# Kernel tuning notes

Measured on AMD Instinct MI355X. Metric: run time of the kernel, lower is better.

Reference implementation:

```python
import jax, jax.numpy as jnp
import numpy as np

N, S, C, E = 32768, 32768, 1024, 16384   # nodes, subgraph-node entries, clusters (=B*P), coarsen edges
F, D, B, P, NC = 64, 64, 16, 64, 10      # feat dim, hidden, graphs, patches per graph, classes


def setup_inputs():
    key = jax.random.key(0)
    ks = list(jax.random.split(key, 24))
    p = lambda k, shp: jax.random.normal(k, shp, dtype=jnp.float32) * 0.05
    z = lambda n: jnp.zeros((n,), jnp.float32)
    return {
        "x": jax.random.normal(ks[0], (N, F), dtype=jnp.float32),
        "subgraphs_nodes_mapper": jax.random.randint(ks[1], (S,), 0, N, dtype=jnp.int32),
        "subgraphs_batch": jnp.sort(jax.random.randint(ks[2], (S,), 0, C, dtype=jnp.int32)),
        "subgraphs_batch_row": jax.random.randint(ks[3], (E,), 0, C, dtype=jnp.int32),
        "subgraphs_batch_col": jax.random.randint(ks[4], (E,), 0, C, dtype=jnp.int32),
        "coarsen_edge_attr": jax.random.uniform(ks[5], (E,), dtype=jnp.float32),
        "W_in1": p(ks[6], (F, D)), "b_in1": z(D),
        "W_in2": p(ks[7], (D, D)), "b_in2": z(D),
        "W_pre1": p(ks[8], (D, D)), "b_pre1": z(D),
        "W_pre2": p(ks[9], (D, D)), "b_pre2": z(D),
        "W_post1": p(ks[10], (D, D)), "b_post1": z(D),
        "W_post2": p(ks[11], (D, D)), "b_post2": z(D),
        "W_K": p(ks[12], (D, D)), "b_K": z(D),
        "W_V": p(ks[13], (D, D)), "b_V": z(D),
        "alpha_beta": jax.random.normal(ks[14], (2,), dtype=jnp.float32),
        "W_c1": p(ks[15], (D, D // 2)), "b_c1": z(D // 2),
        "W_c2": p(ks[16], (D // 2, NC)), "b_c2": z(NC),
    }


def reference(x, subgraphs_nodes_mapper, subgraphs_batch, subgraphs_batch_row,
              subgraphs_batch_col, coarsen_edge_attr,
              W_in1, b_in1, W_in2, b_in2, W_pre1, b_pre1, W_pre2, b_pre2,
              W_post1, b_post1, W_post2, b_post2, W_K, b_K, W_V, b_V,
              alpha_beta, W_c1, b_c1, W_c2, b_c2):
    seg_sum = lambda v, idx: jax.ops.segment_sum(v, idx, num_segments=C)
    # input transform MLP (use_gnn=False path)
    h = jax.nn.relu(x @ W_in1 + b_in1)
    h = jax.nn.relu(h @ W_in2 + b_in2)
    sx = h[subgraphs_nodes_mapper]                        # [S, D] irregular gather
    b = subgraphs_batch
    row, col = subgraphs_batch_row, subgraphs_batch_col
    # bincount-based symmetric degree normalization of coarsened edge weights
    deg = seg_sum(coarsen_edge_attr, row)                 # [C]
    dinv = jnp.where(deg > 0, deg ** -0.5, 0.0)
    ea = dinv[row] * coarsen_edge_attr * dinv[col]        # [E]
    # Q path: pre-deepset -> scatter sum -> post-deepset
    Q = jax.nn.relu(sx @ W_pre1 + b_pre1) @ W_pre2 + b_pre2
    Qs = seg_sum(Q, b)
    Qs = jax.nn.relu(Qs @ W_post1 + b_post1) @ W_post2 + b_post2  # [C, D]
    # K / V paths
    K = sx @ W_K + b_K                                    # [S, D]
    cnt = jnp.maximum(seg_sum(jnp.ones((S,), sx.dtype), b), 1.0)
    Ks = seg_sum(K, b) / cnt[:, None]                     # scatter-mean [C, D]
    V = sx @ W_V + b_V                                    # [S, D]
    # relu kernelization
    Qk, Kk, Ksk = jax.nn.relu(Qs), jax.nn.relu(K), jax.nn.relu(Ks)
    ab = jax.nn.softmax(alpha_beta)
    sa, sb = ab[0] ** -0.5, ab[1] ** -0.5
    ck = jnp.concatenate([sa * Ksk[b], sb * Kk], axis=-1)   # [S, 2D]
    cq = jnp.concatenate([sa * Qk, sb * Qk], axis=-1)       # [C, 2D] (diffQ=False)
    ck_s = seg_sum(ck, b)                                   # [C, 2D]
    M = ck[:, :, None] * V[:, None, :]                      # [S, 2D, D] per-entry outer product
    Ms = seg_sum(M, b)                                      # [C, 2D, D]
    # Double_Level_MessageProp / KeyProp on coarsened graph: out[c] = sum_e ea_e * x[row_e] at col_e
    Ms = seg_sum(ea[:, None, None] * Ms[row], col)
    ck_s = seg_sum(ea[:, None] * ck_s[row], col)
    H = jnp.einsum('ci,cij->cj', cq, Ms)                    # [C, D]
    den = jnp.sum(cq * ck_s, axis=-1, keepdims=True) + 1e-6
    out = H / den                                           # [C, D]
    g = out.reshape(B, P, D).mean(axis=1)                   # mean readout over patches
    logits = jax.nn.relu(g @ W_c1 + b_c1) @ W_c2 + b_c2     # [B, NC]
    return logits
```

## Files before the change

kernel.cpp:

```cpp
#include <hip/hip_runtime.h>
#include <math.h>

constexpr int NN = 32768;
constexpr int SS = 32768;
constexpr int CC = 1024;
constexpr int EE = 16384;
constexpr int BB = 16;
constexpr int PP = 64;
constexpr int NC = 10;
constexpr int ECAP = 64;

__device__ __forceinline__ float rdlane(float v, int l) {
    return __int_as_float(__builtin_amdgcn_readlane(__float_as_int(v), l));
}

#define TS 68

__device__ __forceinline__ void gemm64(const float* A, const float* W,
                                       const float* __restrict__ bias,
                                       int r0, int c0, float acc[4][4])
{
#pragma unroll
    for (int dc = 0; dc < 4; ++dc) {
        float bv = bias[c0 + dc];
        acc[0][dc] = bv; acc[1][dc] = bv; acc[2][dc] = bv; acc[3][dc] = bv;
    }
#pragma unroll 16
    for (int k = 0; k < 64; ++k) {
        float4 av = *(const float4*)(A + k * TS + r0);
        float4 wv = *(const float4*)(W + k * TS + c0);
        acc[0][0] = fmaf(av.x, wv.x, acc[0][0]); acc[0][1] = fmaf(av.x, wv.y, acc[0][1]);
        acc[0][2] = fmaf(av.x, wv.z, acc[0][2]); acc[0][3] = fmaf(av.x, wv.w, acc[0][3]);
        acc[1][0] = fmaf(av.y, wv.x, acc[1][0]); acc[1][1] = fmaf(av.y, wv.y, acc[1][1]);
        acc[1][2] = fmaf(av.y, wv.z, acc[1][2]); acc[1][3] = fmaf(av.y, wv.w, acc[1][3]);
        acc[2][0] = fmaf(av.z, wv.x, acc[2][0]); acc[2][1] = fmaf(av.z, wv.y, acc[2][1]);
        acc[2][2] = fmaf(av.z, wv.z, acc[2][2]); acc[2][3] = fmaf(av.z, wv.w, acc[2][3]);
        acc[3][0] = fmaf(av.w, wv.x, acc[3][0]); acc[3][1] = fmaf(av.w, wv.y, acc[3][1]);
        acc[3][2] = fmaf(av.w, wv.z, acc[3][2]); acc[3][3] = fmaf(av.w, wv.w, acc[3][3]);
    }
}

__device__ __forceinline__ void gemm64x3(const float* A, const float* Wa,
                                         const float* Wb, const float* Wc_,
                                         const float* __restrict__ b1_,
                                         const float* __restrict__ b2_,
                                         const float* __restrict__ b3_,
                                         int r0, int c0,
                                         float a1_[4][4], float a2_[4][4], float a3_[4][4])
{
#pragma unroll
    for (int dc = 0; dc < 4; ++dc) {
        float v1 = b1_[c0 + dc], v2 = b2_[c0 + dc], v3 = b3_[c0 + dc];
#pragma unroll
        for (int dr = 0; dr < 4; ++dr) { a1_[dr][dc] = v1; a2_[dr][dc] = v2; a3_[dr][dc] = v3; }
    }
#pragma unroll 4
    for (int k = 0; k < 64; ++k) {
        float4 av = *(const float4*)(A + k * TS + r0);
        float4 w1 = *(const float4*)(Wa + k * TS + c0);
        float4 w2 = *(const float4*)(Wb + k * TS + c0);
        float4 w3 = *(const float4*)(Wc_ + k * TS + c0);
        float ar[4] = {av.x, av.y, av.z, av.w};
        float u1[4] = {w1.x, w1.y, w1.z, w1.w};
        float u2[4] = {w2.x, w2.y, w2.z, w2.w};
        float u3[4] = {w3.x, w3.y, w3.z, w3.w};
#pragma unroll
        for (int dr = 0; dr < 4; ++dr)
#pragma unroll
            for (int dc = 0; dc < 4; ++dc) {
                a1_[dr][dc] = fmaf(ar[dr], u1[dc], a1_[dr][dc]);
                a2_[dr][dc] = fmaf(ar[dr], u2[dc], a2_[dr][dc]);
                a3_[dr][dc] = fmaf(ar[dr], u3[dc], a3_[dr][dc]);
            }
    }
}

__device__ __forceinline__ void writeW(float* dst, int tid,
                                       float4 a, float4 b, float4 c, float4 d)
{
    int colq = (tid & 15) * 4;
    int rb = tid >> 4;
    *(float4*)(dst + (rb     ) * TS + colq) = a;
    *(float4*)(dst + (rb + 16) * TS + colq) = b;
    *(float4*)(dst + (rb + 32) * TS + colq) = c;
    *(float4*)(dst + (rb + 48) * TS + colq) = d;
}

__device__ __forceinline__ void writeXT(float* dst, int tid,
                                        float4 a, float4 b, float4 c, float4 d)
{
    int rb = (tid * 4) & 63;
    int cb = tid >> 4;
    dst[(rb + 0) * TS + cb     ] = a.x;
    dst[(rb + 1) * TS + cb     ] = a.y;
    dst[(rb + 2) * TS + cb     ] = a.z;
    dst[(rb + 3) * TS + cb     ] = a.w;
    dst[(rb + 0) * TS + cb + 16] = b.x;
    dst[(rb + 1) * TS + cb + 16] = b.y;
    dst[(rb + 2) * TS + cb + 16] = b.z;
    dst[(rb + 3) * TS + cb + 16] = b.w;
    dst[(rb + 0) * TS + cb + 32] = c.x;
    dst[(rb + 1) * TS + cb + 32] = c.y;
    dst[(rb + 2) * TS + cb + 32] = c.z;
    dst[(rb + 3) * TS + cb + 32] = c.w;
    dst[(rb + 0) * TS + cb + 48] = d.x;
    dst[(rb + 1) * TS + cb + 48] = d.y;
    dst[(rb + 2) * TS + cb + 48] = d.z;
    dst[(rb + 3) * TS + cb + 48] = d.w;
}

__device__ __forceinline__ void outT_relu(float* dst, int r0, int c0, float acc[4][4])
{
#pragma unroll
    for (int dc = 0; dc < 4; ++dc) {
        *(float4*)(dst + (c0 + dc) * TS + r0) =
            make_float4(fmaxf(acc[0][dc], 0.f), fmaxf(acc[1][dc], 0.f),
                        fmaxf(acc[2][dc], 0.f), fmaxf(acc[3][dc], 0.f));
    }
}

__device__ __forceinline__ void outG2(float* __restrict__ dst, size_t rowbase, int ld,
                                      int off, int r0, int c0, float acc[4][4], bool dorelu)
{
#pragma unroll
    for (int dr = 0; dr < 4; ++dr) {
        float4 v = make_float4(acc[dr][0], acc[dr][1], acc[dr][2], acc[dr][3]);
        if (dorelu) {
            v.x = fmaxf(v.x, 0.f); v.y = fmaxf(v.y, 0.f);
            v.z = fmaxf(v.z, 0.f); v.w = fmaxf(v.w, 0.f);
        }
        *(float4*)(dst + (rowbase + r0 + dr) * ld + off + c0) = v;
    }
}

__global__ __launch_bounds__(256, 2) void k_node(
    const float* __restrict__ x,
    const int* __restrict__ row, const float* __restrict__ attr,
    const int* __restrict__ batch,
    const float* __restrict__ W1, const float* __restrict__ b1,
    const float* __restrict__ W2, const float* __restrict__ b2,
    const float* __restrict__ Wp1, const float* __restrict__ bp1,
    const float* __restrict__ WK, const float* __restrict__ bK,
    const float* __restrict__ WV, const float* __restrict__ bV,
    float* __restrict__ u, float* __restrict__ KV,
    float* __restrict__ deg, int* __restrict__ segoff,
    int* __restrict__ gcnt, int* __restrict__ ebuck,
    float* __restrict__ zbase)
{
    __shared__ __align__(16) float bufA[64 * TS];
    __shared__ __align__(16) float bufB[64 * TS];
    __shared__ __align__(16) float w0[64 * TS];
    __shared__ __align__(16) float w1[64 * TS];
    __shared__ float ldeg[16];
    __shared__ int lbk[4];
    int tid = threadIdx.x;
    int b = blockIdx.x;
    if (tid < 33) {
        int i = b * 33 + tid;
        if (i < 16640) ((float4*)zbase)[i] = make_float4(0.f, 0.f, 0.f, 0.f);
    }
    if (b < 64) {
        if (tid < 16) ldeg[tid] = 0.f;
        __syncthreads();
        int lo = b * 16;
#pragma unroll 4
        for (int i = 0; i < 64; ++i) {
            int e = i * 256 + tid;
            int r = row[e];
            unsigned d = (unsigned)(r - lo);
            if (d < 16u) atomicAdd(&ldeg[d], attr[e]);
        }
        __syncthreads();
        if (tid < 16) deg[lo + tid] = ldeg[tid];
    } else if (b < 192) {
        int t = (b - 64) * 256 + tid;
        int cur = batch[t];
        int prev = (t == 0) ? -1 : batch[t - 1];
        for (int c = prev + 1; c <= cur; ++c) segoff[c] = t;
        if (t == SS - 1)
            for (int c = cur + 1; c <= CC; ++c) segoff[c] = SS;
    } else if (b < 448) {
        int crow = (b - 192) * 4;
        if (tid < 4) lbk[tid] = 0;
        __syncthreads();
#pragma unroll 4
        for (int i = 0; i < 64; ++i) {
            int e = i * 256 + tid;
            int r = row[e];
            unsigned d = (unsigned)(r - crow);
            if (d < 4u) {
                int pos = atomicAdd(&lbk[d], 1);
                if (pos < ECAP) ebuck[(size_t)(crow + d) * ECAP + pos] = e;
            }
        }
        __syncthreads();
        if (tid < 4) gcnt[crow + tid] = min(lbk[tid], ECAP);
    }
    int tx = tid & 15, ty = tid >> 4;
    int r0 = ty * 4, c0 = tx * 4;
    size_t rowbase = (size_t)b * 64;
    const float* xb = x + rowbase * 64;
    float4 a0 = ((const float4*)W1)[tid];
    float4 a1 = ((const float4*)W1)[tid + 256];
    float4 a2 = ((const float4*)W1)[tid + 512];
    float4 a3 = ((const float4*)W1)[tid + 768];
    float4 x0 = ((const float4*)xb)[tid];
    float4 x1 = ((const float4*)xb)[tid + 256];
    float4 x2 = ((const float4*)xb)[tid + 512];
    float4 x3 = ((const float4*)xb)[tid + 768];
    writeW(w0, tid, a0, a1, a2, a3);
    writeXT(bufA, tid, x0, x1, x2, x3);
    __syncthreads();
    float acc[4][4];
    a0 = ((const float4*)W2)[tid];
    a1 = ((const float4*)W2)[tid + 256];
    a2 = ((const float4*)W2)[tid + 512];
    a3 = ((const float4*)W2)[tid + 768];
    gemm64(bufA, w0, b1, r0, c0, acc);
    outT_relu(bufB, r0, c0, acc);
    writeW(w1, tid, a0, a1, a2, a3);
    __syncthreads();
    a0 = ((const float4*)Wp1)[tid];
    a1 = ((const float4*)Wp1)[tid + 256];
    a2 = ((const float4*)Wp1)[tid + 512];
    a3 = ((const float4*)Wp1)[tid + 768];
    float4 k0 = ((const float4*)WK)[tid];
    float4 k1 = ((const float4*)WK)[tid + 256];
    float4 k2 = ((const float4*)WK)[tid + 512];
    float4 k3 = ((const float4*)WK)[tid + 768];
    float4 v0 = ((const float4*)WV)[tid];
    float4 v1 = ((const float4*)WV)[tid + 256];
    float4 v2 = ((const float4*)WV)[tid + 512];
    float4 v3 = ((const float4*)WV)[tid + 768];
    gemm64(bufB, w1, b2, r0, c0, acc);
    outT_relu(bufA, r0, c0, acc);
    writeW(w0, tid, a0, a1, a2, a3);
    writeW(w1, tid, k0, k1, k2, k3);
    writeW(bufB, tid, v0, v1, v2, v3);
    __syncthreads();
    float accU[4][4], accK[4][4], accV[4][4];
    gemm64x3(bufA, w0, w1, bufB, bp1, bK, bV, r0, c0, accU, accK, accV);
    outG2(u, rowbase, 64, 0, r0, c0, accU, true);
    outG2(KV, rowbase, 128, 0, r0, c0, accK, false);
    outG2(KV, rowbase, 128, 64, r0, c0, accV, false);
}

__global__ __launch_bounds__(256, 4) void k_qk(
    const float* __restrict__ u, const int* __restrict__ mapper,
    const int* __restrict__ segoff,
    const float* __restrict__ Wp2, const float* __restrict__ bp2,
    const float* __restrict__ Wpo1, const float* __restrict__ bpo1,
    const float* __restrict__ Wpo2, const float* __restrict__ bpo2,
    float* __restrict__ Qk)
{
    __shared__ float accs[4][64];
    int c = blockIdx.x;
    int tid = threadIdx.x, j = tid & 63, g = tid >> 6;
    int s0 = segoff[c], s1 = segoff[c + 1];
    float L = (float)(s1 - s0);
    if (tid < 64) {
        accs[0][tid] = 0.f;
        accs[1][tid] = L * bp2[tid];
        accs[2][tid] = bpo1[tid];
        accs[3][tid] = bpo2[tid];
    }
    __syncthreads();
    float us = 0.f;
    for (int s = s0 + g; s < s1; s += 4) us += u[(size_t)mapper[s] * 64 + j];
    atomicAdd(&accs[0][j], us);
    __syncthreads();
    float usv = accs[0][j];
    float p = 0.f;
#pragma unroll
    for (int t = 0; t < 16; ++t) {
        int i = g * 16 + t;
        p = fmaf(rdlane(usv, i), Wp2[i * 64 + j], p);
    }
    atomicAdd(&accs[1][j], p);
    __syncthreads();
    float qs = accs[1][j];
    p = 0.f;
#pragma unroll
    for (int t = 0; t < 16; ++t) {
        int i = g * 16 + t;
        p = fmaf(rdlane(qs, i), Wpo1[i * 64 + j], p);
    }
    atomicAdd(&accs[2][j], p);
    __syncthreads();
    float tv = fmaxf(accs[2][j], 0.f);
    p = 0.f;
#pragma unroll
    for (int t = 0; t < 16; ++t) {
        int i = g * 16 + t;
        p = fmaf(rdlane(tv, i), Wpo2[i * 64 + j], p);
    }
    atomicAdd(&accs[3][j], p);
    __syncthreads();
    if (g == 0) Qk[c * 64 + j] = fmaxf(accs[3][j], 0.f);
}

#define KSTR 72
#define MSTR 68

__global__ __launch_bounds__(256, 4) void k_msbedge(
    const float* __restrict__ KV, const int* __restrict__ mapper,
    const int* __restrict__ segoff, const float* __restrict__ Qk,
    const int* __restrict__ col, const float* __restrict__ attr,
    const float* __restrict__ deg,
    const int* __restrict__ gcnt, const int* __restrict__ ebuck,
    const float* __restrict__ ab,
    float* __restrict__ H, float* __restrict__ den)
{
    __shared__ __align__(16) float Kr[32 * KSTR];
    __shared__ __align__(16) float Vb[32 * KSTR];
    __shared__ __align__(16) float msb[64 * MSTR];
    __shared__ int map_lds[32];
    __shared__ float sums[192];
    __shared__ float dvec[64];
    __shared__ int ecol[ECAP];
    __shared__ float ewt[ECAP];
    int c = blockIdx.x;
    int tid = threadIdx.x, j = tid & 63, g = tid >> 6;
    int tx = tid & 15, ty = tid >> 4;
    int r0 = ty * 4, c0 = tx * 4;
    int ne = gcnt[c];
    if (ne == 0) return;
    int nr = (ne + 15) & ~15;
    if (tid < 192) sums[tid] = 0.f;
    if (tid < ne) {
        int e = ebuck[(size_t)c * ECAP + tid];
        int cd = col[e];
        float dc = deg[cd];
        float dinvc = dc > 0.f ? 1.f / sqrtf(dc) : 0.f;
        float drr = deg[c];
        float dinvr = drr > 0.f ? 1.f / sqrtf(drr) : 0.f;
        ecol[tid] = cd;
        ewt[tid] = dinvr * attr[e] * dinvc;
    }
    for (int p = ne + tid; p < nr; p += 256) { ecol[p] = c; ewt[p] = 0.f; }
    int s0 = segoff[c], s1 = segoff[c + 1];
    float acc[4][4];
#pragma unroll
    for (int a = 0; a < 4; ++a)
#pragma unroll
        for (int bq = 0; bq < 4; ++bq) acc[a][bq] = 0.f;
    float ks = 0.f, krs = 0.f, vs = 0.f;
    for (int sb = s0; sb < s1; sb += 32) {
        int clen = min(32, s1 - sb);
        __syncthreads();
        if (tid < clen) map_lds[tid] = mapper[sb + tid];
        __syncthreads();
        for (int p = tid; p < clen * 32; p += 256) {
            int e = p >> 5, q = p & 31;
            int m = map_lds[e];
            float4 v = *(const float4*)(KV + (size_t)m * 128 + q * 4);
            float* dst = (q < 16) ? &Kr[e * KSTR + q * 4] : &Vb[e * KSTR + (q - 16) * 4];
            *(float4*)dst = v;
        }
        __syncthreads();
#pragma unroll 4
        for (int s = 0; s < clen; ++s) {
            float4 a4 = *(const float4*)(&Kr[s * KSTR + r0]);
            float4 b4 = *(const float4*)(&Vb[s * KSTR + c0]);
            float ar0 = fmaxf(a4.x, 0.f), ar1 = fmaxf(a4.y, 0.f);
            float ar2 = fmaxf(a4.z, 0.f), ar3 = fmaxf(a4.w, 0.f);
            acc[0][0] = fmaf(ar0, b4.x, acc[0][0]); acc[0][1] = fmaf(ar0, b4.y, acc[0][1]);
            acc[0][2] = fmaf(ar0, b4.z, acc[0][2]); acc[0][3] = fmaf(ar0, b4.w, acc[0][3]);
            acc[1][0] = fmaf(ar1, b4.x, acc[1][0]); acc[1][1] = fmaf(ar1, b4.y, acc[1][1]);
            acc[1][2] = fmaf(ar1, b4.z, acc[1][2]); acc[1][3] = fmaf(ar1, b4.w, acc[1][3]);
            acc[2][0] = fmaf(ar2, b4.x, acc[2][0]); acc[2][1] = fmaf(ar2, b4.y, acc[2][1]);
            acc[2][2] = fmaf(ar2, b4.z, acc[2][2]); acc[2][3] = fmaf(ar2, b4.w, acc[2][3]);
            acc[3][0] = fmaf(ar3, b4.x, acc[3][0]); acc[3][1] = fmaf(ar3, b4.y, acc[3][1]);
            acc[3][2] = fmaf(ar3, b4.z, acc[3][2]); acc[3][3] = fmaf(ar3, b4.w, acc[3][3]);
        }
        for (int s = g; s < clen; s += 4) {
            float kv = Kr[s * KSTR + j];
            ks += kv;
            krs += fmaxf(kv, 0.f);
            vs += Vb[s * KSTR + j];
        }
    }
    atomicAdd(&sums[j], ks);
    atomicAdd(&sums[64 + j], krs);
    atomicAdd(&sums[128 + j], vs);
    __syncthreads();
    int L = s1 - s0;
    float Lr = (float)L;
    float invLm = 1.f / (float)(L > 0 ? L : 1);
    float a0 = ab[0], a1 = ab[1];
    float sa2 = 1.f + expf(a1 - a0);
    float sb2 = 1.f + expf(a0 - a1);
    if (tid < 64) {
        float kskv = fmaxf(sums[tid] * invLm, 0.f);
        dvec[tid] = sa2 * Lr * kskv + sb2 * sums[64 + tid];
    }
    float4 vsl4 = *(const float4*)(&sums[128 + c0]);
#pragma unroll
    for (int a = 0; a < 4; ++a) {
        float kska = fmaxf(sums[r0 + a] * invLm, 0.f) * sa2;
        *(float4*)(&msb[(r0 + a) * MSTR + c0]) =
            make_float4(fmaf(kska, vsl4.x, sb2 * acc[a][0]),
                        fmaf(kska, vsl4.y, sb2 * acc[a][1]),
                        fmaf(kska, vsl4.z, sb2 * acc[a][2]),
                        fmaf(kska, vsl4.w, sb2 * acc[a][3]));
    }
    __syncthreads();
    float dvreg = dvec[j];
    int m0 = g * 4;
    if (m0 >= nr) return;
    int cd0 = ecol[m0 + 0], cd1 = ecol[m0 + 1];
    int cd2 = ecol[m0 + 2], cd3 = ecol[m0 + 3];
    float wt0 = ewt[m0 + 0], wt1 = ewt[m0 + 1];
    float wt2 = ewt[m0 + 2], wt3 = ewt[m0 + 3];
    float q0 = Qk[(size_t)cd0 * 64 + j];
    float q1 = Qk[(size_t)cd1 * 64 + j];
    float q2 = Qk[(size_t)cd2 * 64 + j];
    float q3 = Qk[(size_t)cd3 * 64 + j];
    for (; m0 < nr; ) {
        int n0 = m0 + 16;
        int ncd0 = 0, ncd1 = 0, ncd2 = 0, ncd3 = 0;
        float nwt0 = 0.f, nwt1 = 0.f, nwt2 = 0.f, nwt3 = 0.f;
        float nq0 = 0.f, nq1 = 0.f, nq2 = 0.f, nq3 = 0.f;
        if (n0 < nr) {
            ncd0 = ecol[n0 + 0]; ncd1 = ecol[n0 + 1];
            ncd2 = ecol[n0 + 2]; ncd3 = ecol[n0 + 3];
            nwt0 = ewt[n0 + 0]; nwt1 = ewt[n0 + 1];
            nwt2 = ewt[n0 + 2]; nwt3 = ewt[n0 + 3];
            nq0 = Qk[(size_t)ncd0 * 64 + j];
            nq1 = Qk[(size_t)ncd1 * 64 + j];
            nq2 = Qk[(size_t)ncd2 * 64 + j];
            nq3 = Qk[(size_t)ncd3 * 64 + j];
        }
        float o0 = 0.f, o1 = 0.f, o2 = 0.f, o3 = 0.f;
#pragma unroll
        for (int i = 0; i < 64; ++i) {
            float mv = msb[i * MSTR + j];
            o0 = fmaf(rdlane(q0, i), mv, o0);
            o1 = fmaf(rdlane(q1, i), mv, o1);
            o2 = fmaf(rdlane(q2, i), mv, o2);
            o3 = fmaf(rdlane(q3, i), mv, o3);
        }
        float p0 = q0 * dvreg, p1 = q1 * dvreg, p2 = q2 * dvreg, p3 = q3 * dvreg;
#pragma unroll
        for (int o = 32; o > 0; o >>= 1) {
            p0 += __shfl_xor(p0, o);
            p1 += __shfl_xor(p1, o);
            p2 += __shfl_xor(p2, o);
            p3 += __shfl_xor(p3, o);
        }
        atomicAdd(&H[(size_t)cd0 * 64 + j], wt0 * o0);
        atomicAdd(&H[(size_t)cd1 * 64 + j], wt1 * o1);
        atomicAdd(&H[(size_t)cd2 * 64 + j], wt2 * o2);
        atomicAdd(&H[(size_t)cd3 * 64 + j], wt3 * o3);
        if (j == 0) {
            atomicAdd(&den[cd0], wt0 * p0);
            atomicAdd(&den[cd1], wt1 * p1);
            atomicAdd(&den[cd2], wt2 * p2);
            atomicAdd(&den[cd3], wt3 * p3);
        }
        m0 = n0;
        cd0 = ncd0; cd1 = ncd1; cd2 = ncd2; cd3 = ncd3;
        wt0 = nwt0; wt1 = nwt1; wt2 = nwt2; wt3 = nwt3;
        q0 = nq0; q1 = nq1; q2 = nq2; q3 = nq3;
    }
}

__global__ __launch_bounds__(64) void k_final(
    const float* __restrict__ H, const float* __restrict__ den,
    const float* __restrict__ Wc1, const float* __restrict__ bc1,
    const float* __restrict__ Wc2, const float* __restrict__ bc2,
    float* __restrict__ out)
{
    int bg = blockIdx.x;
    int j = threadIdx.x;
    float acc = 0.f;
    for (int p = 0; p < PP; ++p) {
        int c = bg * PP + p;
        acc += H[c * 64 + j] / (den[c] + 1e-6f);
    }
    float g = acc * (1.f / (float)PP);
    int m = j & 31;
    float a1 = bc1[m];
#pragma unroll
    for (int i = 0; i < 64; ++i) a1 = fmaf(rdlane(g, i), Wc1[i * 32 + m], a1);
    float c1 = fmaxf(a1, 0.f);
    int n = (j < NC) ? j : 0;
    float a2 = bc2[n];
#pragma unroll
    for (int i = 0; i < 32; ++i) a2 = fmaf(rdlane(c1, i), Wc2[i * NC + n], a2);
    if (j < NC) out[bg * NC + j] = a2;
}

extern "C" void kernel_launch(void* const* d_in, const int* in_sizes, int n_in,
                              void* d_out, int out_size, void* d_ws, size_t ws_size,
                              hipStream_t stream)
{
    const float* x      = (const float*)d_in[0];
    const int*   mapper = (const int*)d_in[1];
    const int*   batch  = (const int*)d_in[2];
    const int*   row    = (const int*)d_in[3];
    const int*   col    = (const int*)d_in[4];
    const float* attr   = (const float*)d_in[5];
    const float* W_in1  = (const float*)d_in[6];
    const float* b_in1  = (const float*)d_in[7];
    const float* W_in2  = (const float*)d_in[8];
    const float* b_in2  = (const float*)d_in[9];
    const float* W_pre1 = (const float*)d_in[10];
    const float* b_pre1 = (const float*)d_in[11];
    const float* W_pre2 = (const float*)d_in[12];
    const float* b_pre2 = (const float*)d_in[13];
    const float* W_post1= (const float*)d_in[14];
    const float* b_post1= (const float*)d_in[15];
    const float* W_post2= (const float*)d_in[16];
    const float* b_post2= (const float*)d_in[17];
    const float* W_K    = (const float*)d_in[18];
    const float* b_K    = (const float*)d_in[19];
    const float* W_V    = (const float*)d_in[20];
    const float* b_V    = (const float*)d_in[21];
    const float* alpha_beta = (const float*)d_in[22];
    const float* W_c1   = (const float*)d_in[23];
    const float* b_c1   = (const float*)d_in[24];
    const float* W_c2   = (const float*)d_in[25];
    const float* b_c2   = (const float*)d_in[26];

    float* ws = (float*)d_ws;
    float* u     = ws;
    float* KV    = u     + (size_t)NN * 64;
    float* Qk    = KV    + (size_t)NN * 128;
    float* deg   = Qk    + (size_t)CC * 64;
    float* H     = deg   + (size_t)CC;
    float* den   = H     + (size_t)CC * 64;
    int*  segoff = (int*)(den + (size_t)CC);
    int*  gcnt   = segoff + (CC + 1);
    int*  ebuck  = gcnt + CC;

    k_node<<<NN / 64, 256, 0, stream>>>(x, row, attr, batch,
                                        W_in1, b_in1, W_in2, b_in2,
                                        W_pre1, b_pre1, W_K, b_K, W_V, b_V,
                                        u, KV, deg, segoff, gcnt, ebuck, H);
    k_qk<<<CC, 256, 0, stream>>>(u, mapper, segoff, W_pre2, b_pre2,
                                 W_post1, b_post1, W_post2, b_post2, Qk);
    k_msbedge<<<CC, 256, 0, stream>>>(KV, mapper, segoff, Qk, col, attr,
                                      deg, gcnt, ebuck, alpha_beta, H, den);
    k_final<<<BB, 64, 0, stream>>>(H, den, W_c1, b_c1, W_c2, b_c2, (float*)d_out);
}
```

Baseline: 90.21 us.

## Double node-MLP tile to 128 rows per block with 8x4 register tiles

The node-MLP kernel now handles 128 rows per block, so each thread computes 8x4 outputs instead of 4x4. Weight tiles are reused across more rows and the launch uses half as many blocks. The side tasks (zero-fill, edge bucketing over 16 rows per block) are redistributed to match the smaller grid. Shared buffers are reorganised to free one weight buffer, at the cost of extra barriers. Launch bounds drop to one block per SIMD, so the higher register use reduces occupancy and wave count, which on 256 blocks may underfill the GPU.

```diff
diff --git a/kernel.cpp b/kernel.cpp
--- a/kernel.cpp
+++ b/kernel.cpp
@@ -14,58 +14,61 @@
     return __int_as_float(__builtin_amdgcn_readlane(__float_as_int(v), l));
 }
 
+#define AS 136
 #define TS 68
 
-__device__ __forceinline__ void gemm64(const float* A, const float* W,
+__device__ __forceinline__ void gemm84(const float* A, const float* W,
                                        const float* __restrict__ bias,
-                                       int r0, int c0, float acc[4][4])
+                                       int r0, int c0, float acc[8][4])
 {
 #pragma unroll
     for (int dc = 0; dc < 4; ++dc) {
         float bv = bias[c0 + dc];
-        acc[0][dc] = bv; acc[1][dc] = bv; acc[2][dc] = bv; acc[3][dc] = bv;
-    }
-#pragma unroll 16
+#pragma unroll
+        for (int dr = 0; dr < 8; ++dr) acc[dr][dc] = bv;
+    }
+#pragma unroll 8
     for (int k = 0; k < 64; ++k) {
-        float4 av = *(const float4*)(A + k * TS + r0);
+        float4 a0 = *(const float4*)(A + k * AS + r0);
+        float4 a1 = *(const float4*)(A + k * AS + r0 + 4);
         float4 wv = *(const float4*)(W + k * TS + c0);
-        acc[0][0] = fmaf(av.x, wv.x, acc[0][0]); acc[0][1] = fmaf(av.x, wv.y, acc[0][1]);
-        acc[0][2] = fmaf(av.x, wv.z, acc[0][2]); acc[0][3] = fmaf(av.x, wv.w, acc[0][3]);
-        acc[1][0] = fmaf(av.y, wv.x, acc[1][0]); acc[1][1] = fmaf(av.y, wv.y, acc[1][1]);
-        acc[1][2] = fmaf(av.y, wv.z, acc[1][2]); acc[1][3] = fmaf(av.y, wv.w, acc[1][3]);
-        acc[2][0] = fmaf(av.z, wv.x, acc[2][0]); acc[2][1] = fmaf(av.z, wv.y, acc[2][1]);
-        acc[2][2] = fmaf(av.z, wv.z, acc[2][2]); acc[2][3] = fmaf(av.z, wv.w, acc[2][3]);
-        acc[3][0] = fmaf(av.w, wv.x, acc[3][0]); acc[3][1] = fmaf(av.w, wv.y, acc[3][1]);
-        acc[3][2] = fmaf(av.w, wv.z, acc[3][2]); acc[3][3] = fmaf(av.w, wv.w, acc[3][3]);
-    }
-}
-
-__device__ __forceinline__ void gemm64x3(const float* A, const float* Wa,
+        float ar[8] = {a0.x, a0.y, a0.z, a0.w, a1.x, a1.y, a1.z, a1.w};
+        float wr[4] = {wv.x, wv.y, wv.z, wv.w};
+#pragma unroll
+        for (int dr = 0; dr < 8; ++dr)
+#pragma unroll
+            for (int dc = 0; dc < 4; ++dc)
+                acc[dr][dc] = fmaf(ar[dr], wr[dc], acc[dr][dc]);
+    }
+}
+
+__device__ __forceinline__ void gemm84x3(const float* A, const float* Wa,
                                          const float* Wb, const float* Wc_,
                                          const float* __restrict__ b1_,
                                          const float* __restrict__ b2_,
                                          const float* __restrict__ b3_,
                                          int r0, int c0,
-                                         float a1_[4][4], float a2_[4][4], float a3_[4][4])
+                                         float a1_[8][4], float a2_[8][4], float a3_[8][4])
 {
 #pragma unroll
     for (int dc = 0; dc < 4; ++dc) {
         float v1 = b1_[c0 + dc], v2 = b2_[c0 + dc], v3 = b3_[c0 + dc];
 #pragma unroll
-        for (int dr = 0; dr < 4; ++dr) { a1_[dr][dc] = v1; a2_[dr][dc] = v2; a3_[dr][dc] = v3; }
+        for (int dr = 0; dr < 8; ++dr) { a1_[dr][dc] = v1; a2_[dr][dc] = v2; a3_[dr][dc] = v3; }
     }
 #pragma unroll 4
     for (int k = 0; k < 64; ++k) {
-        float4 av = *(const float4*)(A + k * TS + r0);
+        float4 a0 = *(const float4*)(A + k * AS + r0);
+        float4 a1 = *(const float4*)(A + k * AS + r0 + 4);
         float4 w1 = *(const float4*)(Wa + k * TS + c0);
         float4 w2 = *(const float4*)(Wb + k * TS + c0);
         float4 w3 = *(const float4*)(Wc_ + k * TS + c0);
-        float ar[4] = {av.x, av.y, av.z, av.w};
+        float ar[8] = {a0.x, a0.y, a0.z, a0.w, a1.x, a1.y, a1.z, a1.w};
         float u1[4] = {w1.x, w1.y, w1.z, w1.w};
         float u2[4] = {w2.x, w2.y, w2.z, w2.w};
         float u3[4] = {w3.x, w3.y, w3.z, w3.w};
 #pragma unroll
-        for (int dr = 0; dr < 4; ++dr)
+        for (int dr = 0; dr < 8; ++dr)
 #pragma unroll
             for (int dc = 0; dc < 4; ++dc) {
                 a1_[dr][dc] = fmaf(ar[dr], u1[dc], a1_[dr][dc]);
@@ -86,44 +89,32 @@
     *(float4*)(dst + (rb + 48) * TS + colq) = d;
 }
 
-__device__ __forceinline__ void writeXT(float* dst, int tid,
-                                        float4 a, float4 b, float4 c, float4 d)
-{
-    int rb = (tid * 4) & 63;
-    int cb = tid >> 4;
-    dst[(rb + 0) * TS + cb     ] = a.x;
-    dst[(rb + 1) * TS + cb     ] = a.y;
-    dst[(rb + 2) * TS + cb     ] = a.z;
-    dst[(rb + 3) * TS + cb     ] = a.w;
-    dst[(rb + 0) * TS + cb + 16] = b.x;
-    dst[(rb + 1) * TS + cb + 16] = b.y;
-    dst[(rb + 2) * TS + cb + 16] = b.z;
-    dst[(rb + 3) * TS + cb + 16] = b.w;
-    dst[(rb + 0) * TS + cb + 32] = c.x;
-    dst[(rb + 1) * TS + cb + 32] = c.y;
-    dst[(rb + 2) * TS + cb + 32] = c.z;
-    dst[(rb + 3) * TS + cb + 32] = c.w;
-    dst[(rb + 0) * TS + cb + 48] = d.x;
-    dst[(rb + 1) * TS + cb + 48] = d.y;
-    dst[(rb + 2) * TS + cb + 48] = d.z;
-    dst[(rb + 3) * TS + cb + 48] = d.w;
-}
-
-__device__ __forceinline__ void outT_relu(float* dst, int r0, int c0, float acc[4][4])
+__device__ __forceinline__ void writeXT1(float* dst, int rw, int cb, float4 v)
+{
+    dst[(cb + 0) * AS + rw] = v.x;
+    dst[(cb + 1) * AS + rw] = v.y;
+    dst[(cb + 2) * AS + rw] = v.z;
+    dst[(cb + 3) * AS + rw] = v.w;
+}
+
+__device__ __forceinline__ void outT8_relu(float* dst, int r0, int c0, float acc[8][4])
 {
 #pragma unroll
     for (int dc = 0; dc < 4; ++dc) {
-        *(float4*)(dst + (c0 + dc) * TS + r0) =
+        *(float4*)(dst + (c0 + dc) * AS + r0) =
             make_float4(fmaxf(acc[0][dc], 0.f), fmaxf(acc[1][dc], 0.f),
                         fmaxf(acc[2][dc], 0.f), fmaxf(acc[3][dc], 0.f));
-    }
-}
-
-__device__ __forceinline__ void outG2(float* __restrict__ dst, size_t rowbase, int ld,
-                                      int off, int r0, int c0, float acc[4][4], bool dorelu)
-{
-#pragma unroll
-    for (int dr = 0; dr < 4; ++dr) {
+        *(float4*)(dst + (c0 + dc) * AS + r0 + 4) =
+            make_float4(fmaxf(acc[4][dc], 0.f), fmaxf(acc[5][dc], 0.f),
+                        fmaxf(acc[6][dc], 0.f), fmaxf(acc[7][dc], 0.f));
+    }
+}
+
+__device__ __forceinline__ void outG8(float* __restrict__ dst, size_t rowbase, int ld,
+                                      int off, int r0, int c0, float acc[8][4], bool dorelu)
+{
+#pragma unroll
+    for (int dr = 0; dr < 8; ++dr) {
         float4 v = make_float4(acc[dr][0], acc[dr][1], acc[dr][2], acc[dr][3]);
         if (dorelu) {
             v.x = fmaxf(v.x, 0.f); v.y = fmaxf(v.y, 0.f);
@@ -133,7 +124,7 @@
     }
 }
 
-__global__ __launch_bounds__(256, 2) void k_node(
+__global__ __launch_bounds__(256, 1) void k_node(
     const float* __restrict__ x,
     const int* __restrict__ row, const float* __restrict__ attr,
     const int* __restrict__ batch,
@@ -147,16 +138,15 @@
     int* __restrict__ gcnt, int* __restrict__ ebuck,
     float* __restrict__ zbase)
 {
-    __shared__ __align__(16) float bufA[64 * TS];
-    __shared__ __align__(16) float bufB[64 * TS];
+    __shared__ __align__(16) float bufA[64 * AS];
+    __shared__ __align__(16) float bufB[64 * AS];
     __shared__ __align__(16) float w0[64 * TS];
-    __shared__ __align__(16) float w1[64 * TS];
     __shared__ float ldeg[16];
-    __shared__ int lbk[4];
+    __shared__ int lbk[16];
     int tid = threadIdx.x;
     int b = blockIdx.x;
-    if (tid < 33) {
-        int i = b * 33 + tid;
+    if (tid < 65) {
+        int i = b * 65 + tid;
         if (i < 16640) ((float4*)zbase)[i] = make_float4(0.f, 0.f, 0.f, 0.f);
     }
     if (b < 64) {
@@ -179,46 +169,61 @@
         for (int c = prev + 1; c <= cur; ++c) segoff[c] = t;
         if (t == SS - 1)
             for (int c = cur + 1; c <= CC; ++c) segoff[c] = SS;
-    } else if (b < 448) {
-        int crow = (b - 192) * 4;
-        if (tid < 4) lbk[tid] = 0;
+    } else {
+        int crow = (b - 192) * 16;
+        if (tid < 16) lbk[tid] = 0;
         __syncthreads();
 #pragma unroll 4
         for (int i = 0; i < 64; ++i) {
             int e = i * 256 + tid;
             int r = row[e];
             unsigned d = (unsigned)(r - crow);
-            if (d < 4u) {
+            if (d < 16u) {
                 int pos = atomicAdd(&lbk[d], 1);
                 if (pos < ECAP) ebuck[(size_t)(crow + d) * ECAP + pos] = e;
             }
         }
         __syncthreads();
-        if (tid < 4) gcnt[crow + tid] = min(lbk[tid], ECAP);
+        if (tid < 16) gcnt[crow + tid] = min(lbk[tid], ECAP);
     }
     int tx = tid & 15, ty = tid >> 4;
-    int r0 = ty * 4, c0 = tx * 4;
-    size_t rowbase = (size_t)b * 64;
+    int r0 = ty * 8, c0 = tx * 4;
+    size_t rowbase = (size_t)b * 128;
     const float* xb = x + rowbase * 64;
+    float4 x0 = ((const float4*)xb)[tid];
+    float4 x1 = ((const float4*)xb)[tid + 256];
+    float4 x2 = ((const float4*)xb)[tid + 512];
+    float4 x3 = ((const float4*)xb)[tid + 768];
+    float4 x4 = ((const float4*)xb)[tid + 1024];
+    float4 x5 = ((const float4*)xb)[tid + 1280];
+    float4 x6 = ((const float4*)xb)[tid + 1536];
+    float4 x7 = ((const float4*)xb)[tid + 1792];
     float4 a0 = ((const float4*)W1)[tid];
     float4 a1 = ((const float4*)W1)[tid + 256];
     float4 a2 = ((const float4*)W1)[tid + 512];
     float4 a3 = ((const float4*)W1)[tid + 768];
-    float4 x0 = ((const float4*)xb)[tid];
-    float4 x1 = ((const float4*)xb)[tid + 256];
-    float4 x2 = ((const float4*)xb)[tid + 512];
-    float4 x3 = ((const float4*)xb)[tid + 768];
+    {
+        int rw = tid >> 4, cb = (tid & 15) * 4;
+        writeXT1(bufA, rw      , cb, x0);
+        writeXT1(bufA, rw +  16, cb, x1);
+        writeXT1(bufA, rw +  32, cb, x2);
+        writeXT1(bufA, rw +  48, cb, x3);
+        writeXT1(bufA, rw +  64, cb, x4);
+        writeXT1(bufA, rw +  80, cb, x5);
+        writeXT1(bufA, rw +  96, cb, x6);
+        writeXT1(bufA, rw + 112, cb, x7);
+    }
     writeW(w0, tid, a0, a1, a2, a3);
-    writeXT(bufA, tid, x0, x1, x2, x3);
-    __syncthreads();
-    float acc[4][4];
+    __syncthreads();
+    float acc[8][4];
     a0 = ((const float4*)W2)[tid];
     a1 = ((const float4*)W2)[tid + 256];
     a2 = ((const float4*)W2)[tid + 512];
     a3 = ((const float4*)W2)[tid + 768];
-    gemm64(bufA, w0, b1, r0, c0, acc);
-    outT_relu(bufB, r0, c0, acc);
-    writeW(w1, tid, a0, a1, a2, a3);
+    gemm84(bufA, w0, b1, r0, c0, acc);
+    outT8_relu(bufB, r0, c0, acc);
+    __syncthreads();
+    writeW(w0, tid, a0, a1, a2, a3);
     __syncthreads();
     a0 = ((const float4*)Wp1)[tid];
     a1 = ((const float4*)Wp1)[tid + 256];
@@ -232,17 +237,18 @@
     float4 v1 = ((const float4*)WV)[tid + 256];
     float4 v2 = ((const float4*)WV)[tid + 512];
     float4 v3 = ((const float4*)WV)[tid + 768];
-    gemm64(bufB, w1, b2, r0, c0, acc);
-    outT_relu(bufA, r0, c0, acc);
+    gemm84(bufB, w0, b2, r0, c0, acc);
+    outT8_relu(bufA, r0, c0, acc);
+    __syncthreads();
     writeW(w0, tid, a0, a1, a2, a3);
-    writeW(w1, tid, k0, k1, k2, k3);
-    writeW(bufB, tid, v0, v1, v2, v3);
-    __syncthreads();
-    float accU[4][4], accK[4][4], accV[4][4];
-    gemm64x3(bufA, w0, w1, bufB, bp1, bK, bV, r0, c0, accU, accK, accV);
-    outG2(u, rowbase, 64, 0, r0, c0, accU, true);
-    outG2(KV, rowbase, 128, 0, r0, c0, accK, false);
-    outG2(KV, rowbase, 128, 64, r0, c0, accV, false);
+    writeW(bufB, tid, k0, k1, k2, k3);
+    writeW(bufB + 64 * TS, tid, v0, v1, v2, v3);
+    __syncthreads();
+    float accU[8][4], accK[8][4], accV[8][4];
+    gemm84x3(bufA, w0, bufB, bufB + 64 * TS, bp1, bK, bV, r0, c0, accU, accK, accV);
+    outG8(u, rowbase, 64, 0, r0, c0, accU, true);
+    outG8(KV, rowbase, 128, 0, r0, c0, accK, false);
+    outG8(KV, rowbase, 128, 64, r0, c0, accV, false);
 }
 
 __global__ __launch_bounds__(256, 4) void k_qk(
@@ -534,10 +540,10 @@
     int*  gcnt   = segoff + (CC + 1);
     int*  ebuck  = gcnt + CC;
 
-    k_node<<<NN / 64, 256, 0, stream>>>(x, row, attr, batch,
-                                        W_in1, b_in1, W_in2, b_in2,
-                                        W_pre1, b_pre1, W_K, b_K, W_V, b_V,
-                                        u, KV, deg, segoff, gcnt, ebuck, H);
+    k_node<<<NN / 128, 256, 0, stream>>>(x, row, attr, batch,
+                                         W_in1, b_in1, W_in2, b_in2,
+                                         W_pre1, b_pre1, W_K, b_K, W_V, b_V,
+                                         u, KV, deg, segoff, gcnt, ebuck, H);
     k_qk<<<CC, 256, 0, stream>>>(u, mapper, segoff, W_pre2, b_pre2,
                                  W_post1, b_post1, W_post2, b_post2, Qk);
     k_msbedge<<<CC, 256, 0, stream>>>(KV, mapper, segoff, Qk, col, attr,
```

New measurement: 96.60 us. 1.07x slower.
